# Optimization experiments

Hardware: AMD Instinct MI355X
Metric: run time of the kernel (lower is better)

Reference implementation:

```python
import jax, jax.numpy as jnp
import numpy as np

B, D, E = 8192, 4096, 64
TOP_K = 2
NOISE_EPSILON = 0.01


def setup_inputs() -> dict:
    key = jax.random.key(0)
    k1, k2, k3, k4 = jax.random.split(key, 4)
    return {
        "x": jax.random.normal(k1, (B, D), dtype=jnp.float32),
        # nn.Linear weights, init std=0.1, no bias; torch stores [out, in]
        "gate_w": jax.random.normal(k2, (E, D), dtype=jnp.float32) * 0.1,
        "noise_gate_w": jax.random.normal(k3, (E, D), dtype=jnp.float32) * 0.1,
        # deterministic stand-in for torch.randn_like(clean_logits)
        "noise": jax.random.normal(k4, (B, E), dtype=jnp.float32),
    }


def reference(x, gate_w, noise_gate_w, noise):
    # clean_logits = x @ W_g^T : [B, E]
    clean_logits = jnp.einsum("bd,ed->be", x, gate_w)
    # training path: noisy logits with softplus-scaled noise
    noise_logits = jnp.einsum("bd,ed->be", x, noise_gate_w)
    noisy_logits = clean_logits + noise * jax.nn.softplus(noise_logits) * NOISE_EPSILON
    # top-k over experts, softmax over the k selected logits
    top_k_logits, top_k_indices = jax.lax.top_k(noisy_logits, TOP_K)  # [B, k]
    top_k_gates = jax.nn.softmax(top_k_logits, axis=-1)
    # scatter back into dense [B, E] gates
    rows = jnp.arange(noisy_logits.shape[0])[:, None]  # [B, 1]
    gates = jnp.zeros_like(noisy_logits).at[rows, top_k_indices].set(top_k_gates)
    load = jax.nn.softmax(clean_logits, axis=-1)
    return (gates, load)
```

## Files before the change

kernel.cpp:

```cpp
#include <hip/hip_runtime.h>
#include <math.h>

#define BB 8192
#define DD 4096
#define EE 64

constexpr float NOISE_EPS = 0.01f;
constexpr int BM = 64;

typedef __attribute__((ext_vector_type(8))) _Float16 f16x8;
typedef __attribute__((ext_vector_type(4))) float    f32x4;

__device__ __forceinline__ void split8(const float4& a, const float4& b,
                                       f16x8& hi, f16x8& mi) {
    float v[8] = {a.x, a.y, a.z, a.w, b.x, b.y, b.z, b.w};
    #pragma unroll
    for (int j = 0; j < 8; ++j) {
        _Float16 h = (_Float16)v[j];
        hi[j] = h;
        mi[j] = (_Float16)(v[j] - (float)h);
    }
}

__device__ __forceinline__ void block_barrier() {
    asm volatile("s_waitcnt lgkmcnt(0)" ::: "memory");
    __builtin_amdgcn_s_barrier();
    __builtin_amdgcn_sched_barrier(0);
    asm volatile("" ::: "memory");
}

__global__ __launch_bounds__(256) void wsplit_pack(
    const float* __restrict__ gw, const float* __restrict__ ngw,
    char* __restrict__ wpk)
{
    const int gid = blockIdx.x * 256 + threadIdx.x;
    const int r   = gid >> 9;
    const int kc  = gid & 511;
    const int k0  = kc * 8;
    const float* src = (r < EE) ? gw + (size_t)r * DD + k0
                                : ngw + (size_t)(r - EE) * DD + k0;
    float4 a = *reinterpret_cast<const float4*>(src);
    float4 b = *reinterpret_cast<const float4*>(src + 4);
    f16x8 hi, mi;
    split8(a, b, hi, mi);
    const int T    = k0 >> 5;
    const int kq   = (k0 >> 3) & 3;
    const int cb   = r >> 4;
    const int lane = kq * 16 + (r & 15);
    char* base = wpk + (size_t)T * 16384;
    *reinterpret_cast<f16x8*>(base + ((cb * 2 + 0) * 64 + lane) * 16) = hi;
    *reinterpret_cast<f16x8*>(base + ((cb * 2 + 1) * 64 + lane) * 16) = mi;
}

template <int SK>
__global__ __launch_bounds__(512, 4) void gating_main(
    const float* __restrict__ x,
    const char*  __restrict__ wpk,
    float* __restrict__ partial)
{
    constexpr int KC   = DD / SK;
    constexpr int NKS  = KC / 64;
    constexpr int GMAX = 2 * NKS - 1;

    __shared__ __align__(1024) char xls[2][16384];

    const int tid  = threadIdx.x;
    const int bid  = blockIdx.x;
    const int sk   = bid & (SK - 1);
    const int row0 = (bid / SK) * BM;
    const int lane = tid & 63;
    const int wv   = tid >> 6;
    const bool producer = (wv < 4);
    const int l15  = lane & 15;
    const int kq   = lane >> 4;

    char* buf0 = (char*)xls[0];
    char* buf1 = (char*)xls[1];

    const int pr = tid >> 2;
    const int ps = tid & 3;
    const float* xg = x + (size_t)(row0 + pr) * DD + sk * KC + ps * 16;
    const int swp   = pr & 7;
    const int wb    = pr * 256;
    const int wo_h0 = wb       + (((2 * ps)     ^ swp) << 4);
    const int wo_m0 = wb + 128 + (((2 * ps)     ^ swp) << 4);
    const int wo_h1 = wb       + (((2 * ps + 1) ^ swp) << 4);
    const int wo_m1 = wb + 128 + (((2 * ps + 1) ^ swp) << 4);

    #define LOADX(t, V0, V1, V2, V3) do {                                      \
        const float* _s = xg + (size_t)(t) * 64;                               \
        V0 = *reinterpret_cast<const float4*>(_s);                             \
        V1 = *reinterpret_cast<const float4*>(_s + 4);                         \
        V2 = *reinterpret_cast<const float4*>(_s + 8);                         \
        V3 = *reinterpret_cast<const float4*>(_s + 12);                        \
    } while (0)

    #define WSPLIT(bp, V0, V1, V2, V3) do {                                    \
        f16x8 _h, _m;                                                          \
        split8(V0, V1, _h, _m);                                                \
        *reinterpret_cast<f16x8*>((bp) + wo_h0) = _h;                          \
        *reinterpret_cast<f16x8*>((bp) + wo_m0) = _m;                          \
        split8(V2, V3, _h, _m);                                                \
        *reinterpret_cast<f16x8*>((bp) + wo_h1) = _h;                          \
        *reinterpret_cast<f16x8*>((bp) + wo_m1) = _m;                          \
    } while (0)

    const int cw = wv - 4;
    int rbase[4], swz[4];
    #pragma unroll
    for (int ms = 0; ms < 4; ++ms) {
        const int r = ms * 16 + l15;
        rbase[ms] = r * 256;
        swz[ms]   = r & 7;
    }
    const char* wpkB = wpk + ((size_t)(sk * NKS * 2) << 14)
                           + ((cw & 3) * 4096) + lane * 16;

    f32x4 acc[4][2];
    #pragma unroll
    for (int ms = 0; ms < 4; ++ms) {
        acc[ms][0] = {0.f, 0.f, 0.f, 0.f};
        acc[ms][1] = {0.f, 0.f, 0.f, 0.f};
    }

    #define LOADB(g, H0, M0, H1, M1) do {                                      \
        const char* _b = wpkB + ((size_t)(g) << 14);                           \
        H0 = *reinterpret_cast<const f16x8*>(_b);                              \
        M0 = *reinterpret_cast<const f16x8*>(_b + 1024);                       \
        H1 = *reinterpret_cast<const f16x8*>(_b + 2048);                       \
        M1 = *reinterpret_cast<const f16x8*>(_b + 3072);                       \
    } while (0)

    #define CHUNK(bufp, gc, H0, M0, H1, M1) do {                               \
        const char* _xb = (bufp);                                              \
        const int _c = (gc) & 1;                                               \
        f16x8 ah[4], am[4];                                                    \
        _Pragma("unroll")                                                      \
        for (int ms = 0; ms < 4; ++ms) {                                       \
            const int so = (((_c << 2) | kq) ^ swz[ms]) << 4;                  \
            ah[ms] = *reinterpret_cast<const f16x8*>(_xb + rbase[ms] + so);    \
            am[ms] = *reinterpret_cast<const f16x8*>(_xb + rbase[ms] + 128 + so);\
        }                                                                      \
        _Pragma("unroll")                                                      \
        for (int ms = 0; ms < 4; ++ms) {                                       \
            acc[ms][0] = __builtin_amdgcn_mfma_f32_16x16x32_f16(ah[ms], H0, acc[ms][0], 0,0,0); \
            acc[ms][1] = __builtin_amdgcn_mfma_f32_16x16x32_f16(ah[ms], H1, acc[ms][1], 0,0,0); \
        }                                                                      \
        _Pragma("unroll")                                                      \
        for (int ms = 0; ms < 4; ++ms) {                                       \
            acc[ms][0] = __builtin_amdgcn_mfma_f32_16x16x32_f16(am[ms], H0, acc[ms][0], 0,0,0); \
            acc[ms][1] = __builtin_amdgcn_mfma_f32_16x16x32_f16(am[ms], H1, acc[ms][1], 0,0,0); \
        }                                                                      \
        _Pragma("unroll")                                                      \
        for (int ms = 0; ms < 4; ++ms) {                                       \
            acc[ms][0] = __builtin_amdgcn_mfma_f32_16x16x32_f16(ah[ms], M0, acc[ms][0], 0,0,0); \
            acc[ms][1] = __builtin_amdgcn_mfma_f32_16x16x32_f16(ah[ms], M1, acc[ms][1], 0,0,0); \
        }                                                                      \
        { const int _g = (gc) + 2;                                             \
          LOADB((_g <= GMAX) ? _g : GMAX, H0, M0, H1, M1); }                   \
    } while (0)

    float4 xa0, xa1, xa2, xa3;
    float4 xb0, xb1, xb2, xb3;
    f16x8 pH0, pM0, pH1, pM1;
    f16x8 qH0, qM0, qH1, qM1;

    if (producer) {
        LOADX(0, xa0, xa1, xa2, xa3);
        WSPLIT(buf0, xa0, xa1, xa2, xa3);
        LOADX(1, xb0, xb1, xb2, xb3);
    } else {
        LOADB(0, pH0, pM0, pH1, pM1);
        LOADB(1, qH0, qM0, qH1, qM1);
    }

    for (int t = 0; t < NKS; t += 2) {
        block_barrier();
        if (producer) {
            if (t + 2 < NKS) LOADX(t + 2, xa0, xa1, xa2, xa3);
            WSPLIT(buf1, xb0, xb1, xb2, xb3);
            if (t + 3 < NKS) LOADX(t + 3, xb0, xb1, xb2, xb3);
        } else {
            CHUNK(buf0, 2 * t,     pH0, pM0, pH1, pM1);
            CHUNK(buf0, 2 * t + 1, qH0, qM0, qH1, qM1);
        }

        block_barrier();
        if (producer) {
            if (t + 2 < NKS) WSPLIT(buf0, xa0, xa1, xa2, xa3);
        } else {
            CHUNK(buf1, 2 * t + 2, pH0, pM0, pH1, pM1);
            CHUNK(buf1, 2 * t + 3, qH0, qM0, qH1, qM1);
        }
    }

    #undef LOADX
    #undef WSPLIT
    #undef LOADB
    #undef CHUNK

    if (!producer) {
        const size_t pbase = ((size_t)sk * BB + row0) * 128;
        #pragma unroll
        for (int ms = 0; ms < 4; ++ms) {
            #pragma unroll
            for (int cb = 0; cb < 2; ++cb) {
                #pragma unroll
                for (int j = 0; j < 4; ++j) {
                    const int r = ms * 16 + kq * 4 + j;
                    const int c = (2 * cw + cb) * 16 + l15;
                    partial[pbase + (size_t)r * 128 + c] = acc[ms][cb][j];
                }
            }
        }
    }
}

template <int SK>
__global__ __launch_bounds__(512) void gating_epi(
    const float* __restrict__ partial,
    const float* __restrict__ noise,
    float* __restrict__ out)
{
    const int tid  = threadIdx.x;
    const int wv   = tid >> 6;
    const int lane = tid & 63;
    const int l15  = lane & 15;
    const int kq   = lane >> 4;
    const int grow = blockIdx.x * 32 + wv * 4 + kq;
    const int s    = l15;

    const float* pb = partial + (size_t)grow * 128 + 4 * s;
    float4 c4 = {0.f,0.f,0.f,0.f}, n4 = {0.f,0.f,0.f,0.f};
    #pragma unroll
    for (int k = 0; k < SK; ++k) {
        const float* p = pb + (size_t)k * BB * 128;
        float4 a = *reinterpret_cast<const float4*>(p);
        float4 b = *reinterpret_cast<const float4*>(p + 64);
        c4.x += a.x; c4.y += a.y; c4.z += a.z; c4.w += a.w;
        n4.x += b.x; n4.y += b.y; n4.z += b.z; n4.w += b.w;
    }

    float4 nz = *reinterpret_cast<const float4*>(noise + (size_t)grow * EE + 4 * s);

    float cc[4] = {c4.x, c4.y, c4.z, c4.w};
    float nl[4] = {n4.x, n4.y, n4.z, n4.w};
    float m1 = -3.4e38f, m2 = -3.4e38f;
    int   i1 = -1, i2 = -1;
    float cmax = -3.4e38f;
    #pragma unroll
    for (int j = 0; j < 4; ++j) {
        const int e = 4 * s + j;
        float sp  = fmaxf(nl[j], 0.0f) + log1pf(expf(-fabsf(nl[j])));
        float nzj = (j == 0) ? nz.x : (j == 1) ? nz.y : (j == 2) ? nz.z : nz.w;
        float vno = fmaf(nzj * sp, NOISE_EPS, cc[j]);
        if (vno > m1)      { m2 = m1; i2 = i1; m1 = vno; i1 = e; }
        else if (vno > m2) { m2 = vno; i2 = e; }
        cmax = fmaxf(cmax, cc[j]);
    }

    #pragma unroll
    for (int m = 1; m < 16; m <<= 1) {
        float b1 = __shfl_xor(m1, m, 16);
        int  bi1 = __shfl_xor(i1, m, 16);
        float b2 = __shfl_xor(m2, m, 16);
        int  bi2 = __shfl_xor(i2, m, 16);
        cmax = fmaxf(cmax, __shfl_xor(cmax, m, 16));

        bool bwin = (b1 > m1) || (b1 == m1 && bi1 < i1);
        float t1; int ti1; float t2; int ti2;
        if (bwin) {
            t1 = b1; ti1 = bi1;
            bool aw = (m1 > b2) || (m1 == b2 && i1 < bi2);
            t2 = aw ? m1 : b2; ti2 = aw ? i1 : bi2;
        } else {
            t1 = m1; ti1 = i1;
            bool bw = (b1 > m2) || (b1 == m2 && bi1 < i2);
            t2 = bw ? b1 : m2; ti2 = bw ? bi1 : i2;
        }
        m1 = t1; i1 = ti1; m2 = t2; i2 = ti2;
    }

    float tq = expf(m2 - m1);
    float p1 = 1.0f / (1.0f + tq);
    float p2 = tq * p1;

    float e0 = expf(cc[0] - cmax);
    float e1 = expf(cc[1] - cmax);
    float e2 = expf(cc[2] - cmax);
    float e3 = expf(cc[3] - cmax);
    float sum = e0 + e1 + e2 + e3;
    #pragma unroll
    for (int m = 1; m < 16; m <<= 1) sum += __shfl_xor(sum, m, 16);
    float inv = 1.0f / sum;

    const int eb = 4 * s;
    float4 gt;
    gt.x = (eb     == i1) ? p1 : (eb     == i2) ? p2 : 0.0f;
    gt.y = (eb + 1 == i1) ? p1 : (eb + 1 == i2) ? p2 : 0.0f;
    gt.z = (eb + 2 == i1) ? p1 : (eb + 2 == i2) ? p2 : 0.0f;
    gt.w = (eb + 3 == i1) ? p1 : (eb + 3 == i2) ? p2 : 0.0f;
    float4 ld = {e0 * inv, e1 * inv, e2 * inv, e3 * inv};

    *reinterpret_cast<float4*>(out + (size_t)grow * EE + eb) = gt;
    *reinterpret_cast<float4*>(out + (size_t)BB * EE + (size_t)grow * EE + eb) = ld;
}

extern "C" void kernel_launch(void* const* d_in, const int* in_sizes, int n_in,
                              void* d_out, int out_size, void* d_ws, size_t ws_size,
                              hipStream_t stream) {
    const float* x     = (const float*)d_in[0];
    const float* gw    = (const float*)d_in[1];
    const float* ngw   = (const float*)d_in[2];
    const float* noise = (const float*)d_in[3];
    float* out = (float*)d_out;

    char*  wpk     = (char*)d_ws;
    float* partial = (float*)(wpk + (size_t)2 * 1024 * 1024);

    const size_t MB = 1024 * 1024;

    hipLaunchKernelGGL(wsplit_pack, dim3(256), dim3(256), 0, stream, gw, ngw, wpk);

    if (ws_size >= 18 * MB) {
        hipLaunchKernelGGL(gating_main<4>, dim3((BB / BM) * 4), dim3(512), 0, stream,
                           x, wpk, partial);
        hipLaunchKernelGGL(gating_epi<4>, dim3(BB / 32), dim3(512), 0, stream,
                           partial, noise, out);
    } else if (ws_size >= 10 * MB) {
        hipLaunchKernelGGL(gating_main<2>, dim3((BB / BM) * 2), dim3(512), 0, stream,
                           x, wpk, partial);
        hipLaunchKernelGGL(gating_epi<2>, dim3(BB / 32), dim3(512), 0, stream,
                           partial, noise, out);
    } else {
        hipLaunchKernelGGL(gating_main<1>, dim3(BB / BM), dim3(512), 0, stream,
                           x, wpk, partial);
        hipLaunchKernelGGL(gating_epi<1>, dim3(BB / 32), dim3(512), 0, stream,
                           partial, noise, out);
    }
}
```

Before: 49.99 us.

## Use two consumer waves with wider 64-column tiles per wave

Consumer waves drop from four to two, and each now computes four 16-column blocks instead of two, so the block shrinks to 384 threads. Each x fragment read from LDS feeds twice as many MFMAs, which cuts LDS read traffic. The B prefetch depth falls from two chunks to one, and one producer global load moves past the second barrier. The cost is more accumulator registers per wave, fewer waves issuing MFMAs per block, and the occupancy hint drops from 4 to 3.

```diff
diff --git a/kernel.cpp b/kernel.cpp
--- a/kernel.cpp
+++ b/kernel.cpp
@@ -53,7 +53,7 @@
 }
 
 template <int SK>
-__global__ __launch_bounds__(512, 4) void gating_main(
+__global__ __launch_bounds__(384, 3) void gating_main(
     const float* __restrict__ x,
     const char*  __restrict__ wpk,
     float* __restrict__ partial)
@@ -114,24 +114,44 @@
         swz[ms]   = r & 7;
     }
     const char* wpkB = wpk + ((size_t)(sk * NKS * 2) << 14)
-                           + ((cw & 3) * 4096) + lane * 16;
-
-    f32x4 acc[4][2];
-    #pragma unroll
-    for (int ms = 0; ms < 4; ++ms) {
-        acc[ms][0] = {0.f, 0.f, 0.f, 0.f};
-        acc[ms][1] = {0.f, 0.f, 0.f, 0.f};
-    }
-
-    #define LOADB(g, H0, M0, H1, M1) do {                                      \
+                           + (cw & 1) * 8192 + lane * 16;
+
+    f32x4 acc[4][4];
+    #pragma unroll
+    for (int ms = 0; ms < 4; ++ms)
+        #pragma unroll
+        for (int cb = 0; cb < 4; ++cb)
+            acc[ms][cb] = {0.f, 0.f, 0.f, 0.f};
+
+    f16x8 bh0, bm0, bh1, bm1, bh2, bm2, bh3, bm3;
+
+    #define LOADB_ALL(g) do {                                                  \
         const char* _b = wpkB + ((size_t)(g) << 14);                           \
-        H0 = *reinterpret_cast<const f16x8*>(_b);                              \
-        M0 = *reinterpret_cast<const f16x8*>(_b + 1024);                       \
-        H1 = *reinterpret_cast<const f16x8*>(_b + 2048);                       \
-        M1 = *reinterpret_cast<const f16x8*>(_b + 3072);                       \
-    } while (0)
-
-    #define CHUNK(bufp, gc, H0, M0, H1, M1) do {                               \
+        bh0 = *reinterpret_cast<const f16x8*>(_b);                             \
+        bm0 = *reinterpret_cast<const f16x8*>(_b + 1024);                      \
+        bh1 = *reinterpret_cast<const f16x8*>(_b + 2048);                      \
+        bm1 = *reinterpret_cast<const f16x8*>(_b + 3072);                      \
+        bh2 = *reinterpret_cast<const f16x8*>(_b + 4096);                      \
+        bm2 = *reinterpret_cast<const f16x8*>(_b + 5120);                      \
+        bh3 = *reinterpret_cast<const f16x8*>(_b + 6144);                      \
+        bm3 = *reinterpret_cast<const f16x8*>(_b + 7168);                      \
+    } while (0)
+
+    #define CBBLK(CB, H, M) do {                                               \
+        _Pragma("unroll")                                                      \
+        for (int ms = 0; ms < 4; ++ms)                                         \
+            acc[ms][CB] = __builtin_amdgcn_mfma_f32_16x16x32_f16(ah[ms], H, acc[ms][CB], 0,0,0); \
+        _Pragma("unroll")                                                      \
+        for (int ms = 0; ms < 4; ++ms)                                         \
+            acc[ms][CB] = __builtin_amdgcn_mfma_f32_16x16x32_f16(am[ms], H, acc[ms][CB], 0,0,0); \
+        _Pragma("unroll")                                                      \
+        for (int ms = 0; ms < 4; ++ms)                                         \
+            acc[ms][CB] = __builtin_amdgcn_mfma_f32_16x16x32_f16(ah[ms], M, acc[ms][CB], 0,0,0); \
+        H = *reinterpret_cast<const f16x8*>(_nb + (2 * (CB)) * 1024);          \
+        M = *reinterpret_cast<const f16x8*>(_nb + (2 * (CB) + 1) * 1024);      \
+    } while (0)
+
+    #define CHUNK(bufp, gc) do {                                               \
         const char* _xb = (bufp);                                              \
         const int _c = (gc) & 1;                                               \
         f16x8 ah[4], am[4];                                                    \
@@ -141,37 +161,23 @@
             ah[ms] = *reinterpret_cast<const f16x8*>(_xb + rbase[ms] + so);    \
             am[ms] = *reinterpret_cast<const f16x8*>(_xb + rbase[ms] + 128 + so);\
         }                                                                      \
-        _Pragma("unroll")                                                      \
-        for (int ms = 0; ms < 4; ++ms) {                                       \
-            acc[ms][0] = __builtin_amdgcn_mfma_f32_16x16x32_f16(ah[ms], H0, acc[ms][0], 0,0,0); \
-            acc[ms][1] = __builtin_amdgcn_mfma_f32_16x16x32_f16(ah[ms], H1, acc[ms][1], 0,0,0); \
-        }                                                                      \
-        _Pragma("unroll")                                                      \
-        for (int ms = 0; ms < 4; ++ms) {                                       \
-            acc[ms][0] = __builtin_amdgcn_mfma_f32_16x16x32_f16(am[ms], H0, acc[ms][0], 0,0,0); \
-            acc[ms][1] = __builtin_amdgcn_mfma_f32_16x16x32_f16(am[ms], H1, acc[ms][1], 0,0,0); \
-        }                                                                      \
-        _Pragma("unroll")                                                      \
-        for (int ms = 0; ms < 4; ++ms) {                                       \
-            acc[ms][0] = __builtin_amdgcn_mfma_f32_16x16x32_f16(ah[ms], M0, acc[ms][0], 0,0,0); \
-            acc[ms][1] = __builtin_amdgcn_mfma_f32_16x16x32_f16(ah[ms], M1, acc[ms][1], 0,0,0); \
-        }                                                                      \
-        { const int _g = (gc) + 2;                                             \
-          LOADB((_g <= GMAX) ? _g : GMAX, H0, M0, H1, M1); }                   \
+        const int _gn = ((gc) + 1 <= GMAX) ? (gc) + 1 : GMAX;                  \
+        const char* _nb = wpkB + ((size_t)_gn << 14);                          \
+        CBBLK(0, bh0, bm0);                                                    \
+        CBBLK(1, bh1, bm1);                                                    \
+        CBBLK(2, bh2, bm2);                                                    \
+        CBBLK(3, bh3, bm3);                                                    \
     } while (0)
 
     float4 xa0, xa1, xa2, xa3;
     float4 xb0, xb1, xb2, xb3;
-    f16x8 pH0, pM0, pH1, pM1;
-    f16x8 qH0, qM0, qH1, qM1;
 
     if (producer) {
         LOADX(0, xa0, xa1, xa2, xa3);
         WSPLIT(buf0, xa0, xa1, xa2, xa3);
         LOADX(1, xb0, xb1, xb2, xb3);
     } else {
-        LOADB(0, pH0, pM0, pH1, pM1);
-        LOADB(1, qH0, qM0, qH1, qM1);
+        LOADB_ALL(0);
     }
 
     for (int t = 0; t < NKS; t += 2) {
@@ -179,24 +185,25 @@
         if (producer) {
             if (t + 2 < NKS) LOADX(t + 2, xa0, xa1, xa2, xa3);
             WSPLIT(buf1, xb0, xb1, xb2, xb3);
-            if (t + 3 < NKS) LOADX(t + 3, xb0, xb1, xb2, xb3);
         } else {
-            CHUNK(buf0, 2 * t,     pH0, pM0, pH1, pM1);
-            CHUNK(buf0, 2 * t + 1, qH0, qM0, qH1, qM1);
+            CHUNK(buf0, 2 * t);
+            CHUNK(buf0, 2 * t + 1);
         }
 
         block_barrier();
         if (producer) {
+            if (t + 3 < NKS) LOADX(t + 3, xb0, xb1, xb2, xb3);
             if (t + 2 < NKS) WSPLIT(buf0, xa0, xa1, xa2, xa3);
         } else {
-            CHUNK(buf1, 2 * t + 2, pH0, pM0, pH1, pM1);
-            CHUNK(buf1, 2 * t + 3, qH0, qM0, qH1, qM1);
+            CHUNK(buf1, 2 * t + 2);
+            CHUNK(buf1, 2 * t + 3);
         }
     }
 
     #undef LOADX
     #undef WSPLIT
-    #undef LOADB
+    #undef LOADB_ALL
+    #undef CBBLK
     #undef CHUNK
 
     if (!producer) {
@@ -204,11 +211,11 @@
         #pragma unroll
         for (int ms = 0; ms < 4; ++ms) {
             #pragma unroll
-            for (int cb = 0; cb < 2; ++cb) {
+            for (int cb = 0; cb < 4; ++cb) {
                 #pragma unroll
                 for (int j = 0; j < 4; ++j) {
                     const int r = ms * 16 + kq * 4 + j;
-                    const int c = (2 * cw + cb) * 16 + l15;
+                    const int c = (4 * cw + cb) * 16 + l15;
                     partial[pbase + (size_t)r * 128 + c] = acc[ms][cb][j];
                 }
             }
@@ -323,17 +330,17 @@
     hipLaunchKernelGGL(wsplit_pack, dim3(256), dim3(256), 0, stream, gw, ngw, wpk);
 
     if (ws_size >= 18 * MB) {
-        hipLaunchKernelGGL(gating_main<4>, dim3((BB / BM) * 4), dim3(512), 0, stream,
+        hipLaunchKernelGGL(gating_main<4>, dim3((BB / BM) * 4), dim3(384), 0, stream,
                            x, wpk, partial);
         hipLaunchKernelGGL(gating_epi<4>, dim3(BB / 32), dim3(512), 0, stream,
                            partial, noise, out);
     } else if (ws_size >= 10 * MB) {
-        hipLaunchKernelGGL(gating_main<2>, dim3((BB / BM) * 2), dim3(512), 0, stream,
+        hipLaunchKernelGGL(gating_main<2>, dim3((BB / BM) * 2), dim3(384), 0, stream,
                            x, wpk, partial);
         hipLaunchKernelGGL(gating_epi<2>, dim3(BB / 32), dim3(512), 0, stream,
                            partial, noise, out);
     } else {
-        hipLaunchKernelGGL(gating_main<1>, dim3(BB / BM), dim3(512), 0, stream,
+        hipLaunchKernelGGL(gating_main<1>, dim3(BB / BM), dim3(384), 0, stream,
                            x, wpk, partial);
         hipLaunchKernelGGL(gating_epi<1>, dim3(BB / 32), dim3(512), 0, stream,
                            partial, noise, out);
```

Result: slower. 82.65 us (+65.3%).
